# Kernel optimization log

Hardware: AMD Instinct MI355X
Metric: run time of the kernel (lower is better)

The kernel has to match this reference:

```python
import jax, jax.numpy as jnp
import numpy as np

B, S, D_IN, D_OUT, BLK = 4, 2048, 4096, 4096, 256


def setup_inputs() -> dict:
    key = jax.random.key(0)
    k1, k2, k3, k4 = jax.random.split(key, 4)
    x = jax.random.normal(k1, (B, S, D_IN), dtype=jnp.float32)
    base_weight = jax.random.normal(k2, (D_OUT, D_IN), dtype=jnp.float32) * 0.02
    base_bias = jax.random.normal(k3, (D_OUT,), dtype=jnp.float32) * 0.02
    # c3a kernel: (out_blocks, in_blocks, block_size), 'gaussian' init
    c3a_kernel = jax.random.normal(k4, (D_OUT // BLK, D_IN // BLK, BLK), dtype=jnp.float32)
    return {"x": x, "base_weight": base_weight, "base_bias": base_bias, "c3a_kernel": c3a_kernel}


def block_circular_convolution(x, kernel):
    # x: (..., in_features); kernel: (p, q, b) with in_features = q*b, out = p*b
    b = kernel.shape[-1]
    xr = x.reshape(*x.shape[:-1], -1, b)          # (..., q, b)
    xf = jnp.fft.rfft(xr)                          # (..., q, b//2+1) complex
    kf = jnp.fft.rfft(kernel)                      # (p, q, b//2+1) complex
    yf = jnp.einsum('...qb,pqb->...pb', xf, kf)    # block circulant matvec in freq domain
    y = jnp.fft.irfft(yf, b)                       # (..., p, b)
    return y.reshape(*x.shape[:-1], -1)            # (..., out_features)


def reference(x, base_weight, base_bias, c3a_kernel):
    # base nn.Linear
    result = jnp.einsum('bsd,od->bso', x, base_weight) + base_bias
    # C3A adapter path (computed in float32, matches torch forward)
    delta = block_circular_convolution(x, c3a_kernel) / x.shape[-1]
    return result + delta
```

## Files before the change

### kernel.cpp

```cpp
#include <hip/hip_runtime.h>
#include <hip/hip_bf16.h>

#define BB 4
#define SS 2048
#define DIN 4096
#define DOUT 4096
#define BLKC 256
#define MM (BB * SS)
#define NN DOUT
#define KK DIN

typedef __attribute__((ext_vector_type(8))) short short8;
typedef __attribute__((ext_vector_type(4))) float f32x4;

__device__ static inline unsigned short bf16rne(float f) {
    unsigned int u = __float_as_uint(f);
    u += 0x7FFF + ((u >> 16) & 1);
    return (unsigned short)(u >> 16);
}

__device__ static inline void gload_lds16(const void* g, void* l) {
    __builtin_amdgcn_global_load_lds(
        (const __attribute__((address_space(1))) void*)g,
        (__attribute__((address_space(3))) void*)l, 16, 0, 0);
}

__global__ __launch_bounds__(256) void cvt_x_bf16(const float* __restrict__ x,
                                                  unsigned short* __restrict__ xb) {
    const int idx = blockIdx.x * 256 + threadIdx.x;
    const size_t i8 = (size_t)idx * 8;
    float4 v0 = *(const float4*)(x + i8);
    float4 v1 = *(const float4*)(x + i8 + 4);
    short8 o;
    o[0] = (short)bf16rne(v0.x); o[1] = (short)bf16rne(v0.y);
    o[2] = (short)bf16rne(v0.z); o[3] = (short)bf16rne(v0.w);
    o[4] = (short)bf16rne(v1.x); o[5] = (short)bf16rne(v1.y);
    o[6] = (short)bf16rne(v1.z); o[7] = (short)bf16rne(v1.w);
    *(short8*)(xb + i8) = o;
}

__global__ __launch_bounds__(256) void build_weff(const float* __restrict__ W,
                                                  const float* __restrict__ k3,
                                                  unsigned short* __restrict__ Wb) {
    const int idx = blockIdx.x * 256 + threadIdx.x;
    const size_t i8 = (size_t)idx * 8;
    const int o = (int)(i8 >> 12);
    const int i = (int)(i8 & 4095);
    const int p = o >> 8, t = o & 255;
    const int q = i >> 8, s0 = i & 255;
    const float* kr = k3 + (((p << 4) + q) << 8);
    float4 w0 = *(const float4*)(W + i8);
    float4 w1 = *(const float4*)(W + i8 + 4);
    float v[8] = {w0.x, w0.y, w0.z, w0.w, w1.x, w1.y, w1.z, w1.w};
    short8 out;
    const float inv = 1.0f / (float)DIN;
#pragma unroll
    for (int j = 0; j < 8; ++j) {
        const int kidx = (t - (s0 + j)) & 255;
        out[j] = (short)bf16rne(v[j] + kr[kidx] * inv);
    }
    *(short8*)(Wb + i8) = out;
}

__global__ __launch_bounds__(256, 2) void gemm_bt(const unsigned short* __restrict__ A,
                                                  const unsigned short* __restrict__ Bw,
                                                  const float* __restrict__ bias,
                                                  float* __restrict__ C) {
    __shared__ unsigned short ldsA[128 * 32];
    __shared__ unsigned short ldsB[128 * 32];

    const int tid = threadIdx.x;
    const int nwg = (MM / 128) * (NN / 128);
    const int bid = blockIdx.x;
    const int swz = (bid & 7) * (nwg >> 3) + (bid >> 3);
    const int bm = swz >> 5;
    const int bn = swz & 31;
    const int m0 = bm * 128, n0 = bn * 128;

    const int l = tid & 63, w = tid >> 6;
    const int wm = (w >> 1) * 64, wn = (w & 1) * 64;
    const int lr = l & 15;
    const int lk = (l >> 4) * 8;

    const int rowA = tid >> 2;
    const int col8 = (tid & 3) * 8;
    const unsigned short* gA = A + (size_t)(m0 + rowA) * KK + col8;
    const unsigned short* gB = Bw + (size_t)(n0 + rowA) * KK + col8;
    unsigned short* lA = &ldsA[tid * 8];
    unsigned short* lB = &ldsB[tid * 8];

    f32x4 acc[4][4];
#pragma unroll
    for (int i = 0; i < 4; ++i)
#pragma unroll
        for (int j = 0; j < 4; ++j) acc[i][j] = (f32x4){0.f, 0.f, 0.f, 0.f};

    for (int kt = 0; kt < KK; kt += 32) {
        gload_lds16(gA + kt, lA);
        gload_lds16(gA + (size_t)64 * KK + kt, lA + 64 * 32);
        gload_lds16(gB + kt, lB);
        gload_lds16(gB + (size_t)64 * KK + kt, lB + 64 * 32);
        __syncthreads();

        short8 af[4], bf[4];
#pragma unroll
        for (int mi = 0; mi < 4; ++mi)
            af[mi] = *(const short8*)&ldsA[(wm + mi * 16 + lr) * 32 + lk];
#pragma unroll
        for (int ni = 0; ni < 4; ++ni)
            bf[ni] = *(const short8*)&ldsB[(wn + ni * 16 + lr) * 32 + lk];
#pragma unroll
        for (int mi = 0; mi < 4; ++mi)
#pragma unroll
            for (int ni = 0; ni < 4; ++ni)
                acc[mi][ni] = __builtin_amdgcn_mfma_f32_16x16x32_bf16(
                    af[mi], bf[ni], acc[mi][ni], 0, 0, 0);
        __syncthreads();
    }

#pragma unroll
    for (int ni = 0; ni < 4; ++ni) {
        const int n = n0 + wn + ni * 16 + lr;
        const float bv = bias[n];
#pragma unroll
        for (int mi = 0; mi < 4; ++mi) {
            const int mbase = m0 + wm + mi * 16 + (l >> 4) * 4;
#pragma unroll
            for (int r = 0; r < 4; ++r)
                C[(size_t)(mbase + r) * NN + n] = acc[mi][ni][r] + bv;
        }
    }
}

extern "C" void kernel_launch(void* const* d_in, const int* in_sizes, int n_in,
                              void* d_out, int out_size, void* d_ws, size_t ws_size,
                              hipStream_t stream) {
    const float* x    = (const float*)d_in[0];
    const float* W    = (const float*)d_in[1];
    const float* bias = (const float*)d_in[2];
    const float* k3   = (const float*)d_in[3];
    float* out = (float*)d_out;

    unsigned short* xb = (unsigned short*)d_ws;
    unsigned short* Wb = (unsigned short*)((char*)d_ws + (size_t)64 * 1024 * 1024);

    cvt_x_bf16<<<(MM * KK) / (256 * 8), 256, 0, stream>>>(x, xb);
    build_weff<<<(NN * KK) / (256 * 8), 256, 0, stream>>>(W, k3, Wb);
    gemm_bt<<<(MM / 128) * (NN / 128), 256, 0, stream>>>(xb, Wb, bias, out);
}
```

Measured before the change: 618.2 us.

## Enlarge GEMM tiles to 256x256, add 4-stage LDS pipeline, fuse prep kernels

Moves the bf16 GEMM from 128x128 tiles with 4 waves to 256x256 tiles with 8 waves, each wave computing a 128x64 sub-tile. It adds a 4-buffer LDS ring that prefetches three K-steps ahead, using vmcnt waits and one barrier per step instead of two syncthreads. It also XOR-swizzles the LDS layout to avoid bank conflicts and raises wave priority around the MFMA blocks. The two preprocessing kernels are merged into one launch. The 64 KB-per-buffer LDS use (128 KB total) and the larger accumulator arrays increase occupancy pressure, so the requested two blocks per CU may not fit.

After: 534.5 us. -13.5%, faster.

```diff
diff --git a/kernel.cpp b/kernel.cpp
--- a/kernel.cpp
+++ b/kernel.cpp
@@ -1,22 +1,20 @@
 #include <hip/hip_runtime.h>
 #include <hip/hip_bf16.h>
 
-#define BB 4
-#define SS 2048
-#define DIN 4096
-#define DOUT 4096
-#define BLKC 256
-#define MM (BB * SS)
-#define NN DOUT
-#define KK DIN
+#define MM 8192
+#define NN 4096
+#define KK 4096
+#define BKT 32
+#define NT (KK / BKT)
 
+typedef unsigned short u16;
 typedef __attribute__((ext_vector_type(8))) short short8;
 typedef __attribute__((ext_vector_type(4))) float f32x4;
 
-__device__ static inline unsigned short bf16rne(float f) {
+__device__ static inline u16 bf16rne(float f) {
     unsigned int u = __float_as_uint(f);
     u += 0x7FFF + ((u >> 16) & 1);
-    return (unsigned short)(u >> 16);
+    return (u16)(u >> 16);
 }
 
 __device__ static inline void gload_lds16(const void* g, void* l) {
@@ -25,111 +23,152 @@
         (__attribute__((address_space(3))) void*)l, 16, 0, 0);
 }
 
-__global__ __launch_bounds__(256) void cvt_x_bf16(const float* __restrict__ x,
-                                                  unsigned short* __restrict__ xb) {
-    const int idx = blockIdx.x * 256 + threadIdx.x;
-    const size_t i8 = (size_t)idx * 8;
-    float4 v0 = *(const float4*)(x + i8);
-    float4 v1 = *(const float4*)(x + i8 + 4);
-    short8 o;
-    o[0] = (short)bf16rne(v0.x); o[1] = (short)bf16rne(v0.y);
-    o[2] = (short)bf16rne(v0.z); o[3] = (short)bf16rne(v0.w);
-    o[4] = (short)bf16rne(v1.x); o[5] = (short)bf16rne(v1.y);
-    o[6] = (short)bf16rne(v1.z); o[7] = (short)bf16rne(v1.w);
-    *(short8*)(xb + i8) = o;
+#define CVT_BLOCKS ((MM * KK) / (256 * 8))
+#define WEF_BLOCKS ((NN * KK) / (256 * 8))
+
+__global__ __launch_bounds__(256) void prep(const float* __restrict__ x,
+                                            const float* __restrict__ W,
+                                            const float* __restrict__ k3,
+                                            u16* __restrict__ xb,
+                                            u16* __restrict__ Wb) {
+    const int bx = blockIdx.x;
+    if (bx < CVT_BLOCKS) {
+        const int idx = bx * 256 + threadIdx.x;
+        const size_t i8 = (size_t)idx * 8;
+        float4 v0 = *(const float4*)(x + i8);
+        float4 v1 = *(const float4*)(x + i8 + 4);
+        short8 o;
+        o[0] = (short)bf16rne(v0.x); o[1] = (short)bf16rne(v0.y);
+        o[2] = (short)bf16rne(v0.z); o[3] = (short)bf16rne(v0.w);
+        o[4] = (short)bf16rne(v1.x); o[5] = (short)bf16rne(v1.y);
+        o[6] = (short)bf16rne(v1.z); o[7] = (short)bf16rne(v1.w);
+        *(short8*)(xb + i8) = o;
+    } else {
+        const int idx = (bx - CVT_BLOCKS) * 256 + threadIdx.x;
+        const size_t i8 = (size_t)idx * 8;
+        const int o = (int)(i8 >> 12);
+        const int i = (int)(i8 & 4095);
+        const int p = o >> 8, t = o & 255;
+        const int q = i >> 8, s0 = i & 255;
+        const float* kr = k3 + (((p << 4) + q) << 8);
+        float4 w0 = *(const float4*)(W + i8);
+        float4 w1 = *(const float4*)(W + i8 + 4);
+        float v[8] = {w0.x, w0.y, w0.z, w0.w, w1.x, w1.y, w1.z, w1.w};
+        short8 out;
+        const float inv = 1.0f / (float)KK;
+#pragma unroll
+        for (int j = 0; j < 8; ++j) {
+            const int kidx = (t - (s0 + j)) & 255;
+            out[j] = (short)bf16rne(v[j] + kr[kidx] * inv);
+        }
+        *(short8*)(Wb + i8) = out;
+    }
 }
 
-__global__ __launch_bounds__(256) void build_weff(const float* __restrict__ W,
-                                                  const float* __restrict__ k3,
-                                                  unsigned short* __restrict__ Wb) {
-    const int idx = blockIdx.x * 256 + threadIdx.x;
-    const size_t i8 = (size_t)idx * 8;
-    const int o = (int)(i8 >> 12);
-    const int i = (int)(i8 & 4095);
-    const int p = o >> 8, t = o & 255;
-    const int q = i >> 8, s0 = i & 255;
-    const float* kr = k3 + (((p << 4) + q) << 8);
-    float4 w0 = *(const float4*)(W + i8);
-    float4 w1 = *(const float4*)(W + i8 + 4);
-    float v[8] = {w0.x, w0.y, w0.z, w0.w, w1.x, w1.y, w1.z, w1.w};
-    short8 out;
-    const float inv = 1.0f / (float)DIN;
-#pragma unroll
-    for (int j = 0; j < 8; ++j) {
-        const int kidx = (t - (s0 + j)) & 255;
-        out[j] = (short)bf16rne(v[j] + kr[kidx] * inv);
-    }
-    *(short8*)(Wb + i8) = out;
-}
-
-__global__ __launch_bounds__(256, 2) void gemm_bt(const unsigned short* __restrict__ A,
-                                                  const unsigned short* __restrict__ Bw,
+__global__ __launch_bounds__(512, 2) void gemm_bt(const u16* __restrict__ A,
+                                                  const u16* __restrict__ Bw,
                                                   const float* __restrict__ bias,
                                                   float* __restrict__ C) {
-    __shared__ unsigned short ldsA[128 * 32];
-    __shared__ unsigned short ldsB[128 * 32];
+    __shared__ u16 lA[4][256 * BKT];
+    __shared__ u16 lB[4][256 * BKT];
 
     const int tid = threadIdx.x;
-    const int nwg = (MM / 128) * (NN / 128);
     const int bid = blockIdx.x;
+    const int nwg = (MM / 256) * (NN / 256);
     const int swz = (bid & 7) * (nwg >> 3) + (bid >> 3);
-    const int bm = swz >> 5;
-    const int bn = swz & 31;
-    const int m0 = bm * 128, n0 = bn * 128;
+    const int m0 = (swz >> 4) * 256;
+    const int n0 = (swz & 15) * 256;
 
-    const int l = tid & 63, w = tid >> 6;
-    const int wm = (w >> 1) * 64, wn = (w & 1) * 64;
+    const int l = tid & 63;
+    const int wid = tid >> 6;
+    const int wr = wid >> 2, wc = wid & 3;
+
     const int lr = l & 15;
-    const int lk = (l >> 4) * 8;
+    const int ks8 = ((((l >> 4) ^ (l & 3) ^ ((l >> 2) & 3)) & 3)) * 8;
 
-    const int rowA = tid >> 2;
-    const int col8 = (tid & 3) * 8;
-    const unsigned short* gA = A + (size_t)(m0 + rowA) * KK + col8;
-    const unsigned short* gB = Bw + (size_t)(n0 + rowA) * KK + col8;
-    unsigned short* lA = &ldsA[tid * 8];
-    unsigned short* lB = &ldsB[tid * 8];
+    const int srow = tid >> 2;
+    const int fst = ((tid >> 2) ^ (tid >> 4)) & 3;
+    const int sslot = ((tid & 3) ^ fst) * 8;
+    const u16* gA0 = A  + (size_t)(m0 + srow) * KK + sslot;
+    const u16* gB0 = Bw + (size_t)(n0 + srow) * KK + sslot;
 
-    f32x4 acc[4][4];
+#define STAGE_A(t)  do { const u16* g_ = gA0 + (t) * BKT; \
+        gload_lds16(g_, &lA[(t) & 3][tid * 8]); \
+        gload_lds16(g_ + (size_t)128 * KK, &lA[(t) & 3][4096 + tid * 8]); } while (0)
+#define STAGE_B(t)  do { const u16* g_ = gB0 + (t) * BKT; \
+        gload_lds16(g_, &lB[(t) & 3][tid * 8]); \
+        gload_lds16(g_ + (size_t)128 * KK, &lB[(t) & 3][4096 + tid * 8]); } while (0)
+
+    f32x4 acc[8][4];
 #pragma unroll
-    for (int i = 0; i < 4; ++i)
+    for (int i = 0; i < 8; ++i)
 #pragma unroll
         for (int j = 0; j < 4; ++j) acc[i][j] = (f32x4){0.f, 0.f, 0.f, 0.f};
 
-    for (int kt = 0; kt < KK; kt += 32) {
-        gload_lds16(gA + kt, lA);
-        gload_lds16(gA + (size_t)64 * KK + kt, lA + 64 * 32);
-        gload_lds16(gB + kt, lB);
-        gload_lds16(gB + (size_t)64 * KK + kt, lB + 64 * 32);
-        __syncthreads();
+    STAGE_A(0); STAGE_B(0);
+    STAGE_A(1); STAGE_B(1);
+    STAGE_A(2); STAGE_B(2);
+    asm volatile("s_waitcnt vmcnt(8)" ::: "memory");
+    __builtin_amdgcn_s_barrier();
+    asm volatile("" ::: "memory");
 
-        short8 af[4], bf[4];
+    const int arow = wr * 128 + lr;
+    const int brow = wc * 64 + lr;
+
+    for (int t = 0; t < NT; ++t) {
+        const u16* bufA = lA[t & 3];
+        const u16* bufB = lB[t & 3];
+
+        short8 a0[4], b0[4];
 #pragma unroll
-        for (int mi = 0; mi < 4; ++mi)
-            af[mi] = *(const short8*)&ldsA[(wm + mi * 16 + lr) * 32 + lk];
+        for (int i = 0; i < 4; ++i)
+            a0[i] = *(const short8*)&bufA[(arow + i * 16) * BKT + ks8];
 #pragma unroll
-        for (int ni = 0; ni < 4; ++ni)
-            bf[ni] = *(const short8*)&ldsB[(wn + ni * 16 + lr) * 32 + lk];
+        for (int j = 0; j < 4; ++j)
+            b0[j] = *(const short8*)&bufB[(brow + j * 16) * BKT + ks8];
+        if (t + 3 < NT) STAGE_A(t + 3);
+        __builtin_amdgcn_s_setprio(1);
 #pragma unroll
-        for (int mi = 0; mi < 4; ++mi)
+        for (int i = 0; i < 4; ++i)
 #pragma unroll
-            for (int ni = 0; ni < 4; ++ni)
-                acc[mi][ni] = __builtin_amdgcn_mfma_f32_16x16x32_bf16(
-                    af[mi], bf[ni], acc[mi][ni], 0, 0, 0);
-        __syncthreads();
+            for (int j = 0; j < 4; ++j)
+                acc[i][j] = __builtin_amdgcn_mfma_f32_16x16x32_bf16(a0[i], b0[j], acc[i][j], 0, 0, 0);
+        __builtin_amdgcn_s_setprio(0);
+
+        short8 a1[4];
+#pragma unroll
+        for (int i = 0; i < 4; ++i)
+            a1[i] = *(const short8*)&bufA[(arow + 64 + i * 16) * BKT + ks8];
+        if (t + 3 < NT) STAGE_B(t + 3);
+        __builtin_amdgcn_s_setprio(1);
+#pragma unroll
+        for (int i = 0; i < 4; ++i)
+#pragma unroll
+            for (int j = 0; j < 4; ++j)
+                acc[4 + i][j] = __builtin_amdgcn_mfma_f32_16x16x32_bf16(a1[i], b0[j], acc[4 + i][j], 0, 0, 0);
+        __builtin_amdgcn_s_setprio(0);
+
+        asm volatile("s_waitcnt vmcnt(8)" ::: "memory");
+        __builtin_amdgcn_s_barrier();
+        asm volatile("" ::: "memory");
     }
 
+    const int crow0 = m0 + wr * 128 + (l >> 4) * 4;
+    const int ccol0 = n0 + wc * 64 + lr;
 #pragma unroll
-    for (int ni = 0; ni < 4; ++ni) {
-        const int n = n0 + wn + ni * 16 + lr;
+    for (int j = 0; j < 4; ++j) {
+        const int n = ccol0 + j * 16;
         const float bv = bias[n];
 #pragma unroll
-        for (int mi = 0; mi < 4; ++mi) {
-            const int mbase = m0 + wm + mi * 16 + (l >> 4) * 4;
+        for (int i = 0; i < 8; ++i) {
+            const int mb = crow0 + i * 16;
 #pragma unroll
             for (int r = 0; r < 4; ++r)
-                C[(size_t)(mbase + r) * NN + n] = acc[mi][ni][r] + bv;
+                C[(size_t)(mb + r) * NN + n] = acc[i][j][r] + bv;
         }
     }
+#undef STAGE_A
+#undef STAGE_B
 }
 
 extern "C" void kernel_launch(void* const* d_in, const int* in_sizes, int n_in,
@@ -141,10 +180,9 @@
     const float* k3   = (const float*)d_in[3];
     float* out = (float*)d_out;
 
-    unsigned short* xb = (unsigned short*)d_ws;
-    unsigned short* Wb = (unsigned short*)((char*)d_ws + (size_t)64 * 1024 * 1024);
+    u16* xb = (u16*)d_ws;
+    u16* Wb = (u16*)((char*)d_ws + (size_t)64 * 1024 * 1024);
 
-    cvt_x_bf16<<<(MM * KK) / (256 * 8), 256, 0, stream>>>(x, xb);
-    build_weff<<<(NN * KK) / (256 * 8), 256, 0, stream>>>(W, k3, Wb);
-    gemm_bt<<<(MM / 128) * (NN / 128), 256, 0, stream>>>(xb, Wb, bias, out);
+    prep<<<CVT_BLOCKS + WEF_BLOCKS, 256, 0, stream>>>(x, W, k3, xb, Wb);
+    gemm_bt<<<(MM / 256) * (NN / 256), 512, 0, stream>>>(xb, Wb, bias, out);
 }
```
